# Performance work log

Hardware: AMD Instinct MI355X
Metric: run time of the kernel (lower is better)

The kernel has to match this reference:

```python
import jax, jax.numpy as jnp
import numpy as np

N_NODES = 100000

def sage_conv(x, src, dst, Wl, bl, Wr):
    # mean aggregation of source features at destination nodes
    msg = x[src]                                        # [E, d] gather
    agg = jax.ops.segment_sum(msg, dst, num_segments=N_NODES)
    deg = jax.ops.segment_sum(jnp.ones((src.shape[0],), x.dtype), dst, num_segments=N_NODES)
    agg = agg / jnp.maximum(deg, 1.0)[:, None]
    return agg @ Wl.T + bl + x @ Wr.T


def setup_inputs() -> dict:
    key = jax.random.key(0)
    ks = jax.random.split(key, 8)
    F, H, C = 128, 128, 64
    E = 1600000
    x = jax.random.normal(ks[0], (N_NODES, F), dtype=jnp.float32)
    edge_index = jax.random.randint(ks[1], (2, E), 0, N_NODES, dtype=jnp.int64)
    s = 1.0 / np.sqrt(F)
    return {
        'x': x,
        'edge_index': edge_index,
        'W1l': jax.random.normal(ks[2], (H, F), dtype=jnp.float32) * s,
        'b1': jnp.zeros((H,), jnp.float32),
        'W1r': jax.random.normal(ks[3], (H, F), dtype=jnp.float32) * s,
        'W2l': jax.random.normal(ks[4], (C, H), dtype=jnp.float32) * s,
        'b2': jnp.zeros((C,), jnp.float32),
        'W2r': jax.random.normal(ks[5], (C, H), dtype=jnp.float32) * s,
    }


def reference(x, edge_index, W1l, b1, W1r, W2l, b2, W2r):
    src, dst = edge_index[0], edge_index[1]
    h = sage_conv(x, src, dst, W1l, b1, W1r)
    h = jax.nn.relu(h)
    # dropout is identity at inference (training=False)
    h = sage_conv(h, src, dst, W2l, b2, W2r)
    return jax.nn.log_softmax(h, axis=1)
```

## Files before the change

### kernel.cpp

```cpp
#include <hip/hip_runtime.h>
#include <hip/hip_bf16.h>

#define N_NODES 100000
#define NBUCKET 250
#define BUCKET_W 400
#define BK_EPT 14

typedef __attribute__((ext_vector_type(8))) short short8;
typedef __attribute__((ext_vector_type(8))) unsigned short u16x8;
typedef __attribute__((ext_vector_type(4))) unsigned short u16x4;
typedef __attribute__((ext_vector_type(4))) float floatx4;
typedef __attribute__((ext_vector_type(2))) float floatx2;

__device__ __forceinline__ float b2f(unsigned short u) {
    return __uint_as_float(((unsigned int)u) << 16);
}
__device__ __forceinline__ unsigned short f2b(float f) {
    unsigned int u = __float_as_uint(f);
    unsigned int r = u + 0x7FFFu + ((u >> 16) & 1u);
    return (unsigned short)(r >> 16);
}

__global__ __launch_bounds__(256) void prep_kernel(
    const float* __restrict__ x,
    const float* __restrict__ W1l, const float* __restrict__ W1r,
    const float* __restrict__ W2l, const float* __restrict__ W2r,
    unsigned short* __restrict__ xb, unsigned char* __restrict__ xq,
    unsigned short* __restrict__ Wc1f,
    unsigned short* __restrict__ W2lf, unsigned short* __restrict__ W2rf,
    int* __restrict__ bucketCursor, int pairCap)
{
    int blk = blockIdx.x;
    if (blk < 12500) {
        int tid = blk * 256 + threadIdx.x;
        float4 v = ((const float4*)x)[tid];
        u16x4 o;
        o.x = f2b(v.x); o.y = f2b(v.y); o.z = f2b(v.z); o.w = f2b(v.w);
        ((u16x4*)xb)[tid] = o;
        int p = 0;
        p = __builtin_amdgcn_cvt_pk_fp8_f32(v.x, v.y, p, false);
        p = __builtin_amdgcn_cvt_pk_fp8_f32(v.z, v.w, p, true);
        ((unsigned int*)xq)[tid] = (unsigned int)p;
    } else if (blk < 12692) {
        int tid = (blk - 12500) * 256 + threadIdx.x;
        if (tid < 32768) {
            int j = tid & 7, lane = (tid >> 3) & 63, t = (tid >> 9) & 7, ks = tid >> 12;
            int m = lane & 15, quad = lane >> 4;
            int row = t * 16 + m;
            int k = ks * 32 + quad * 8 + j;
            float v = (k < 128) ? W1l[row * 128 + k] : W1r[row * 128 + (k - 128)];
            Wc1f[tid] = f2b(v);
        } else if (tid < 40960) {
            int idx = tid - 32768;
            int j = idx & 7, lane = (idx >> 3) & 63, t = (idx >> 9) & 3, ks = idx >> 11;
            int m = lane & 15, quad = lane >> 4;
            int row = t * 16 + m;
            int k = ks * 32 + quad * 8 + j;
            W2lf[idx] = f2b(W2l[row * 128 + k]);
        } else if (tid < 49152) {
            int idx = tid - 40960;
            int j = idx & 7, lane = (idx >> 3) & 63, t = (idx >> 9) & 3, ks = idx >> 11;
            int m = lane & 15, quad = lane >> 4;
            int row = t * 16 + m;
            int k = ks * 32 + quad * 8 + j;
            W2rf[idx] = f2b(W2r[row * 128 + k]);
        }
    } else {
        if (threadIdx.x < NBUCKET)
            bucketCursor[threadIdx.x] = threadIdx.x * pairCap;
    }
}

__global__ __launch_bounds__(1024) void bucket_kernel(
    const int* __restrict__ src, const int* __restrict__ dst,
    int* __restrict__ bucketCursor, int2* __restrict__ pairs, int E)
{
    __shared__ int cnt[NBUCKET];
    __shared__ int base[NBUCKET];
    const int EPB = 1024 * BK_EPT;
    int e0 = blockIdx.x * EPB;
    for (int t = threadIdx.x; t < NBUCKET; t += 1024) cnt[t] = 0;
    __syncthreads();

    int es[BK_EPT], ed[BK_EPT], rk[BK_EPT], bk[BK_EPT];
    #pragma unroll
    for (int j = 0; j < BK_EPT; j++) {
        int i = e0 + j * 1024 + threadIdx.x;
        if (i < E) {
            es[j] = src[i];
            ed[j] = dst[i];
            bk[j] = ed[j] / BUCKET_W;
            rk[j] = atomicAdd(&cnt[bk[j]], 1);
        } else {
            bk[j] = -1;
        }
    }
    __syncthreads();
    for (int t = threadIdx.x; t < NBUCKET; t += 1024)
        base[t] = atomicAdd(&bucketCursor[t], cnt[t]);
    __syncthreads();

    #pragma unroll
    for (int j = 0; j < BK_EPT; j++) {
        if (bk[j] >= 0)
            pairs[(size_t)base[bk[j]] + rk[j]] = make_int2(es[j], ed[j]);
    }
}

__global__ __launch_bounds__(1024) void fill_kernel(
    const int2* __restrict__ pairs, const int* __restrict__ bucketCursor,
    int* __restrict__ edge_src, int2* __restrict__ nodeInfo, int pairCap)
{
    __shared__ int hist[BUCKET_W];
    __shared__ int off[BUCKET_W];
    __shared__ int cur[BUCKET_W];
    int b = blockIdx.x;
    int t = threadIdx.x;
    int base = b * pairCap;
    int cnt = bucketCursor[b] - base;
    int node0 = b * BUCKET_W;

    if (t < BUCKET_W) hist[t] = 0;
    __syncthreads();
    for (int i = t; i < cnt; i += 1024)
        atomicAdd(&hist[pairs[base + i].y - node0], 1);
    __syncthreads();

    if (t < BUCKET_W) off[t] = hist[t];
    __syncthreads();
    for (int o = 1; o < BUCKET_W; o <<= 1) {
        int v = 0;
        if (t < BUCKET_W && t >= o) v = off[t - o];
        __syncthreads();
        if (t < BUCKET_W && t >= o) off[t] += v;
        __syncthreads();
    }
    if (t < BUCKET_W) {
        int gb = base + off[t] - hist[t];
        cur[t] = gb;
        nodeInfo[node0 + t] = make_int2(gb, hist[t]);
    }
    __syncthreads();

    for (int i = t; i < cnt; i += 1024) {
        int2 p = pairs[base + i];
        int pos = atomicAdd(&cur[p.y - node0], 1);
        edge_src[pos] = p.x;
    }
}

__global__ __launch_bounds__(256) void gather_fp8_kernel(
    const unsigned char* __restrict__ xq, const int* __restrict__ edge_src,
    const int2* __restrict__ nodeInfo, unsigned short* __restrict__ aggOut)
{
    int tid = blockIdx.x * 256 + threadIdx.x;
    int node = tid >> 3;
    int q = tid & 7;
    int2 info = nodeInfo[node];
    int e = info.x, deg = info.y, end = info.x + deg;
    const uint4* f16 = (const uint4*)xq;

    float acc[16];
    #pragma unroll
    for (int j = 0; j < 16; j++) acc[j] = 0.0f;

    #define ACC16(W)  do {                                                   \
        floatx2 p;                                                           \
        p = __builtin_amdgcn_cvt_pk_f32_fp8((W).x, false); acc[0]+=p.x; acc[1]+=p.y;  \
        p = __builtin_amdgcn_cvt_pk_f32_fp8((W).x, true);  acc[2]+=p.x; acc[3]+=p.y;  \
        p = __builtin_amdgcn_cvt_pk_f32_fp8((W).y, false); acc[4]+=p.x; acc[5]+=p.y;  \
        p = __builtin_amdgcn_cvt_pk_f32_fp8((W).y, true);  acc[6]+=p.x; acc[7]+=p.y;  \
        p = __builtin_amdgcn_cvt_pk_f32_fp8((W).z, false); acc[8]+=p.x; acc[9]+=p.y;  \
        p = __builtin_amdgcn_cvt_pk_f32_fp8((W).z, true);  acc[10]+=p.x; acc[11]+=p.y;\
        p = __builtin_amdgcn_cvt_pk_f32_fp8((W).w, false); acc[12]+=p.x; acc[13]+=p.y;\
        p = __builtin_amdgcn_cvt_pk_f32_fp8((W).w, true);  acc[14]+=p.x; acc[15]+=p.y;\
    } while (0)

    for (; e + 4 <= end; e += 4) {
        int s0 = edge_src[e + 0];
        int s1 = edge_src[e + 1];
        int s2 = edge_src[e + 2];
        int s3 = edge_src[e + 3];
        uint4 w0 = f16[(size_t)s0 * 8 + q];
        uint4 w1 = f16[(size_t)s1 * 8 + q];
        uint4 w2 = f16[(size_t)s2 * 8 + q];
        uint4 w3 = f16[(size_t)s3 * 8 + q];
        ACC16(w0); ACC16(w1); ACC16(w2); ACC16(w3);
    }
    for (; e < end; e++) {
        uint4 w0 = f16[(size_t)edge_src[e] * 8 + q];
        ACC16(w0);
    }
    #undef ACC16

    float inv = (deg > 0) ? 1.0f / (float)deg : 0.0f;
    u16x8 o0, o1;
    #pragma unroll
    for (int j = 0; j < 8; j++) { o0[j] = f2b(acc[j] * inv); o1[j] = f2b(acc[8 + j] * inv); }
    u16x8* op = (u16x8*)(aggOut + (size_t)node * 128 + q * 16);
    op[0] = o0;
    op[1] = o1;
}

__global__ __launch_bounds__(256, 2) void fused_l1_kernel(
    const unsigned short* __restrict__ a1b, const unsigned short* __restrict__ xb,
    const unsigned short* __restrict__ Wc1f, const float* __restrict__ b1,
    const unsigned short* __restrict__ W2lf, const unsigned short* __restrict__ W2rf,
    unsigned char* __restrict__ g2q, unsigned short* __restrict__ r2b)
{
    __shared__ unsigned short h_lds[4][32][136];

    int wave = threadIdx.x >> 6;
    int lane = threadIdx.x & 63;
    int m    = lane & 15;
    int quad = lane >> 4;
    int node0 = blockIdx.x * 128 + wave * 32;

    int n0 = min(node0 + m,      N_NODES - 1);
    int n1 = min(node0 + 16 + m, N_NODES - 1);

    short8 a0[8], a1[8];
    #pragma unroll
    for (int ks = 0; ks < 8; ks++) {
        int k0 = ks * 32 + quad * 8;
        const unsigned short* s = (ks < 4) ? a1b : xb;
        int koff = (ks < 4) ? k0 : (k0 - 128);
        a0[ks] = *(const short8*)(s + (size_t)n0 * 128 + koff);
        a1[ks] = *(const short8*)(s + (size_t)n1 * 128 + koff);
    }

    floatx4 acc[2][8];
    #pragma unroll
    for (int mt = 0; mt < 2; mt++)
        #pragma unroll
        for (int t = 0; t < 8; t++) acc[mt][t] = (floatx4)(0.0f);

    const unsigned short* Wp = Wc1f + (lane << 3);
    short8 bb[2][8];
    #pragma unroll
    for (int t = 0; t < 8; t++)
        bb[0][t] = *(const short8*)(Wp + ((t * 64) << 3));

    #pragma unroll
    for (int ks = 0; ks < 8; ks++) {
        if (ks < 7) {
            #pragma unroll
            for (int t = 0; t < 8; t++)
                bb[(ks + 1) & 1][t] =
                    *(const short8*)(Wp + ((((ks + 1) * 8 + t) * 64) << 3));
        }
        #pragma unroll
        for (int t = 0; t < 8; t++) {
            acc[0][t] = __builtin_amdgcn_mfma_f32_16x16x32_bf16(a0[ks], bb[ks & 1][t], acc[0][t], 0, 0, 0);
            acc[1][t] = __builtin_amdgcn_mfma_f32_16x16x32_bf16(a1[ks], bb[ks & 1][t], acc[1][t], 0, 0, 0);
        }
    }

    #pragma unroll
    for (int t = 0; t < 8; t++) {
        int j = t * 16 + m;
        float bias = b1[j];
        #pragma unroll
        for (int mt = 0; mt < 2; mt++) {
            #pragma unroll
            for (int r = 0; r < 4; r++) {
                int row = mt * 16 + quad * 4 + r;
                h_lds[wave][row][j] = f2b(fmaxf(acc[mt][t][r] + bias, 0.0f));
            }
        }
    }
    asm volatile("s_waitcnt lgkmcnt(0)" ::: "memory");

    short8 h0[4], h1[4];
    #pragma unroll
    for (int ks = 0; ks < 4; ks++) {
        int k0 = ks * 32 + quad * 8;
        h0[ks] = *(const short8*)&h_lds[wave][m][k0];
        h1[ks] = *(const short8*)&h_lds[wave][16 + m][k0];
    }

    floatx4 acc2[2][4], acc3[2][4];
    #pragma unroll
    for (int mt = 0; mt < 2; mt++)
        #pragma unroll
        for (int t = 0; t < 4; t++) { acc2[mt][t] = (floatx4)(0.0f); acc3[mt][t] = (floatx4)(0.0f); }

    const unsigned short* W2lp = W2lf + (lane << 3);
    const unsigned short* W2rp = W2rf + (lane << 3);
    short8 bl2[2][4], br2[2][4];
    #pragma unroll
    for (int t = 0; t < 4; t++) {
        bl2[0][t] = *(const short8*)(W2lp + ((t * 64) << 3));
        br2[0][t] = *(const short8*)(W2rp + ((t * 64) << 3));
    }

    #pragma unroll
    for (int ks = 0; ks < 4; ks++) {
        if (ks < 3) {
            #pragma unroll
            for (int t = 0; t < 4; t++) {
                bl2[(ks + 1) & 1][t] = *(const short8*)(W2lp + ((((ks + 1) * 4 + t) * 64) << 3));
                br2[(ks + 1) & 1][t] = *(const short8*)(W2rp + ((((ks + 1) * 4 + t) * 64) << 3));
            }
        }
        #pragma unroll
        for (int t = 0; t < 4; t++) {
            acc2[0][t] = __builtin_amdgcn_mfma_f32_16x16x32_bf16(h0[ks], bl2[ks & 1][t], acc2[0][t], 0, 0, 0);
            acc2[1][t] = __builtin_amdgcn_mfma_f32_16x16x32_bf16(h1[ks], bl2[ks & 1][t], acc2[1][t], 0, 0, 0);
            acc3[0][t] = __builtin_amdgcn_mfma_f32_16x16x32_bf16(h0[ks], br2[ks & 1][t], acc3[0][t], 0, 0, 0);
            acc3[1][t] = __builtin_amdgcn_mfma_f32_16x16x32_bf16(h1[ks], br2[ks & 1][t], acc3[1][t], 0, 0, 0);
        }
    }

    #pragma unroll
    for (int mt = 0; mt < 2; mt++) {
        #pragma unroll
        for (int r = 0; r < 4; r++) {
            int n = node0 + mt * 16 + quad * 4 + r;
            if (n < N_NODES) {
                int p = 0;
                p = __builtin_amdgcn_cvt_pk_fp8_f32(acc2[mt][0][r], acc2[mt][1][r], p, false);
                p = __builtin_amdgcn_cvt_pk_fp8_f32(acc2[mt][2][r], acc2[mt][3][r], p, true);
                *(unsigned int*)(g2q + (size_t)n * 64 + m * 4) = (unsigned int)p;
                u16x4 rb;
                rb.x = f2b(acc3[mt][0][r]);
                rb.y = f2b(acc3[mt][1][r]);
                rb.z = f2b(acc3[mt][2][r]);
                rb.w = f2b(acc3[mt][3][r]);
                *(u16x4*)(r2b + (size_t)n * 64 + m * 4) = rb;
            }
        }
    }
}

__global__ __launch_bounds__(256) void gather_final_kernel(
    const unsigned char* __restrict__ g2q, const int* __restrict__ edge_src,
    const int2* __restrict__ nodeInfo, const unsigned short* __restrict__ r2b,
    const float* __restrict__ b2, float* __restrict__ out)
{
    int tid = blockIdx.x * 256 + threadIdx.x;
    int node = tid >> 3;
    int q = tid & 7;
    int2 info = nodeInfo[node];
    int e = info.x, deg = info.y, end = info.x + deg;
    const uint2* f8 = (const uint2*)g2q;
    float acc[8];
    #pragma unroll
    for (int j = 0; j < 8; j++) acc[j] = 0.0f;

    #define ACC8(W)  do {                                                    \
        floatx2 p;                                                           \
        p = __builtin_amdgcn_cvt_pk_f32_fp8((W).x, false); acc[0]+=p.x; acc[1]+=p.y; \
        p = __builtin_amdgcn_cvt_pk_f32_fp8((W).x, true);  acc[2]+=p.x; acc[3]+=p.y; \
        p = __builtin_amdgcn_cvt_pk_f32_fp8((W).y, false); acc[4]+=p.x; acc[5]+=p.y; \
        p = __builtin_amdgcn_cvt_pk_f32_fp8((W).y, true);  acc[6]+=p.x; acc[7]+=p.y; \
    } while (0)

    for (; e + 4 <= end; e += 4) {
        int s0 = edge_src[e + 0];
        int s1 = edge_src[e + 1];
        int s2 = edge_src[e + 2];
        int s3 = edge_src[e + 3];
        uint2 v0 = f8[(size_t)s0 * 8 + q];
        uint2 v1 = f8[(size_t)s1 * 8 + q];
        uint2 v2 = f8[(size_t)s2 * 8 + q];
        uint2 v3 = f8[(size_t)s3 * 8 + q];
        ACC8(v0); ACC8(v1); ACC8(v2); ACC8(v3);
    }
    for (; e < end; e++) {
        uint2 v0 = f8[(size_t)edge_src[e] * 8 + q];
        ACC8(v0);
    }
    #undef ACC8

    float inv = (deg > 0) ? 1.0f / (float)deg : 0.0f;

    u16x8 rv = ((const u16x8*)r2b)[tid];

    float2 bb0 = *(const float2*)(b2 + 0  + 2 * q);
    float2 bb1 = *(const float2*)(b2 + 16 + 2 * q);
    float2 bb2 = *(const float2*)(b2 + 32 + 2 * q);
    float2 bb3 = *(const float2*)(b2 + 48 + 2 * q);

    float v[8];
    v[0] = acc[0] * inv + bb0.x + b2f(rv[0]);
    v[1] = acc[1] * inv + bb1.x + b2f(rv[1]);
    v[2] = acc[2] * inv + bb2.x + b2f(rv[2]);
    v[3] = acc[3] * inv + bb3.x + b2f(rv[3]);
    v[4] = acc[4] * inv + bb0.y + b2f(rv[4]);
    v[5] = acc[5] * inv + bb1.y + b2f(rv[5]);
    v[6] = acc[6] * inv + bb2.y + b2f(rv[6]);
    v[7] = acc[7] * inv + bb3.y + b2f(rv[7]);

    float mx = v[0];
    #pragma unroll
    for (int j = 1; j < 8; j++) mx = fmaxf(mx, v[j]);
    mx = fmaxf(mx, __shfl_xor(mx, 1, 64));
    mx = fmaxf(mx, __shfl_xor(mx, 2, 64));
    mx = fmaxf(mx, __shfl_xor(mx, 4, 64));
    float s = 0.0f;
    #pragma unroll
    for (int j = 0; j < 8; j++) s += expf(v[j] - mx);
    s += __shfl_xor(s, 1, 64);
    s += __shfl_xor(s, 2, 64);
    s += __shfl_xor(s, 4, 64);
    float lg = mx + logf(s);

    float* ob = out + (size_t)node * 64 + 2 * q;
    *(float2*)(ob + 0)  = make_float2(v[0] - lg, v[4] - lg);
    *(float2*)(ob + 16) = make_float2(v[1] - lg, v[5] - lg);
    *(float2*)(ob + 32) = make_float2(v[2] - lg, v[6] - lg);
    *(float2*)(ob + 48) = make_float2(v[3] - lg, v[7] - lg);
}

extern "C" void kernel_launch(void* const* d_in, const int* in_sizes, int n_in,
                              void* d_out, int out_size, void* d_ws, size_t ws_size,
                              hipStream_t stream)
{
    const float* x   = (const float*)d_in[0];
    const int*   ei  = (const int*)d_in[1];
    const float* W1l = (const float*)d_in[2];
    const float* b1  = (const float*)d_in[3];
    const float* W1r = (const float*)d_in[4];
    const float* W2l = (const float*)d_in[5];
    const float* b2  = (const float*)d_in[6];
    const float* W2r = (const float*)d_in[7];
    float* out = (float*)d_out;

    int E = in_sizes[1] / 2;
    const int* src = ei;
    const int* dst = ei + E;

    int pairCap = ((E / NBUCKET) * 3 / 2 + 255) / 256 * 256;

    char* ws = (char*)d_ws;
    int*  bucketCursor = (int*)ws;   ws += ((size_t)NBUCKET * 4 + 15) / 16 * 16;
    int2* pairs        = (int2*)ws;  ws += (size_t)NBUCKET * pairCap * 8;
    int*  edge_src     = (int*)ws;   ws += (size_t)NBUCKET * pairCap * 4;
    int2* nodeInfo     = (int2*)ws;  ws += (size_t)N_NODES * 8;
    unsigned short* xb   = (unsigned short*)ws;  ws += (size_t)N_NODES * 128 * 2;
    unsigned char*  xq   = (unsigned char*)ws;   ws += (size_t)N_NODES * 128;
    unsigned short* a1b  = (unsigned short*)ws;  ws += (size_t)N_NODES * 128 * 2;
    unsigned char*  g2q  = (unsigned char*)ws;   ws += (size_t)N_NODES * 64;
    unsigned short* r2b  = (unsigned short*)ws;  ws += (size_t)N_NODES * 64 * 2;
    unsigned short* Wc1f = (unsigned short*)ws;  ws += 128 * 256 * 2;
    unsigned short* W2lf = (unsigned short*)ws;  ws += 64 * 128 * 2;
    unsigned short* W2rf = (unsigned short*)ws;  ws += 64 * 128 * 2;

    prep_kernel<<<12693, 256, 0, stream>>>(
        x, W1l, W1r, W2l, W2r, xb, xq, Wc1f, W2lf, W2rf, bucketCursor, pairCap);

    {
        const int EPB = 1024 * BK_EPT;
        bucket_kernel<<<(E + EPB - 1) / EPB, 1024, 0, stream>>>(
            src, dst, bucketCursor, pairs, E);
    }

    fill_kernel<<<NBUCKET, 1024, 0, stream>>>(
        pairs, bucketCursor, edge_src, nodeInfo, pairCap);

    gather_fp8_kernel<<<(N_NODES * 8) / 256, 256, 0, stream>>>(
        xq, edge_src, nodeInfo, a1b);

    fused_l1_kernel<<<(N_NODES + 127) / 128, 256, 0, stream>>>(
        a1b, xb, Wc1f, b1, W2lf, W2rf, g2q, r2b);

    gather_final_kernel<<<(N_NODES * 8) / 256, 256, 0, stream>>>(
        g2q, edge_src, nodeInfo, r2b, b2, out);
}
```

Before: 257.8 us.

## Sort edges by source stripe within each node and grid-stride gather kernels

The fill kernel now orders each destination node's edge list by source-node stripe (16 stripes of 6250 nodes), using a 6400-key histogram and a two-level prefix scan. The aim is for concurrently running gather threads to touch nearby source rows at the same time and get better L2 locality. Both gather kernels are also turned into grid-stride loops over 3125 tiles with 1024 persistent blocks, so that within each sweep blocks process nodes in a similar stripe order. The cost is a heavier fill kernel with more shared memory and barriers, and less parallelism in the gathers.

```diff
diff --git a/kernel.cpp b/kernel.cpp
--- a/kernel.cpp
+++ b/kernel.cpp
@@ -5,6 +5,10 @@
 #define NBUCKET 250
 #define BUCKET_W 400
 #define BK_EPT 14
+#define NSTRIPE 16
+#define STRIPE_W 6250
+#define GATHER_TILES 3125
+#define GATHER_BLOCKS 1024
 
 typedef __attribute__((ext_vector_type(8))) short short8;
 typedef __attribute__((ext_vector_type(8))) unsigned short u16x8;
@@ -111,40 +115,58 @@
     const int2* __restrict__ pairs, const int* __restrict__ bucketCursor,
     int* __restrict__ edge_src, int2* __restrict__ nodeInfo, int pairCap)
 {
-    __shared__ int hist[BUCKET_W];
-    __shared__ int off[BUCKET_W];
-    __shared__ int cur[BUCKET_W];
+    const int NKEY = BUCKET_W * NSTRIPE;
+    __shared__ int hist[BUCKET_W * NSTRIPE];
+    __shared__ int offx[BUCKET_W * NSTRIPE];
+    __shared__ int psum[1024];
     int b = blockIdx.x;
     int t = threadIdx.x;
     int base = b * pairCap;
     int cnt = bucketCursor[b] - base;
     int node0 = b * BUCKET_W;
 
-    if (t < BUCKET_W) hist[t] = 0;
-    __syncthreads();
-    for (int i = t; i < cnt; i += 1024)
-        atomicAdd(&hist[pairs[base + i].y - node0], 1);
-    __syncthreads();
-
-    if (t < BUCKET_W) off[t] = hist[t];
-    __syncthreads();
-    for (int o = 1; o < BUCKET_W; o <<= 1) {
-        int v = 0;
-        if (t < BUCKET_W && t >= o) v = off[t - o];
-        __syncthreads();
-        if (t < BUCKET_W && t >= o) off[t] += v;
-        __syncthreads();
-    }
-    if (t < BUCKET_W) {
-        int gb = base + off[t] - hist[t];
-        cur[t] = gb;
-        nodeInfo[node0 + t] = make_int2(gb, hist[t]);
-    }
-    __syncthreads();
-
+    for (int k = t; k < NKEY; k += 1024) hist[k] = 0;
+    __syncthreads();
     for (int i = t; i < cnt; i += 1024) {
         int2 p = pairs[base + i];
-        int pos = atomicAdd(&cur[p.y - node0], 1);
+        int key = (p.y - node0) * NSTRIPE + p.x / STRIPE_W;
+        atomicAdd(&hist[key], 1);
+    }
+    __syncthreads();
+
+    int loc[8];
+    int mysum = 0;
+    if (t < 800) {
+        #pragma unroll
+        for (int j = 0; j < 8; j++) { loc[j] = mysum; mysum += hist[t * 8 + j]; }
+    }
+    psum[t] = mysum;
+    __syncthreads();
+    for (int o = 1; o < 1024; o <<= 1) {
+        int v = (t >= o) ? psum[t - o] : 0;
+        __syncthreads();
+        psum[t] += v;
+        __syncthreads();
+    }
+    int texcl = psum[t] - mysum;
+    if (t < 800) {
+        #pragma unroll
+        for (int j = 0; j < 8; j++) offx[t * 8 + j] = texcl + loc[j];
+    }
+    __syncthreads();
+
+    if (t < BUCKET_W) {
+        int beg = offx[t * NSTRIPE];
+        int nxt = (t == BUCKET_W - 1) ? cnt : offx[(t + 1) * NSTRIPE];
+        nodeInfo[node0 + t] = make_int2(base + beg, nxt - beg);
+    }
+    for (int k = t; k < NKEY; k += 1024) hist[k] = base + offx[k];
+    __syncthreads();
+
+    for (int i = t; i < cnt; i += 1024) {
+        int2 p = pairs[base + i];
+        int key = (p.y - node0) * NSTRIPE + p.x / STRIPE_W;
+        int pos = atomicAdd(&hist[key], 1);
         edge_src[pos] = p.x;
     }
 }
@@ -153,53 +175,55 @@
     const unsigned char* __restrict__ xq, const int* __restrict__ edge_src,
     const int2* __restrict__ nodeInfo, unsigned short* __restrict__ aggOut)
 {
-    int tid = blockIdx.x * 256 + threadIdx.x;
-    int node = tid >> 3;
-    int q = tid & 7;
-    int2 info = nodeInfo[node];
-    int e = info.x, deg = info.y, end = info.x + deg;
-    const uint4* f16 = (const uint4*)xq;
-
-    float acc[16];
-    #pragma unroll
-    for (int j = 0; j < 16; j++) acc[j] = 0.0f;
-
-    #define ACC16(W)  do {                                                   \
-        floatx2 p;                                                           \
-        p = __builtin_amdgcn_cvt_pk_f32_fp8((W).x, false); acc[0]+=p.x; acc[1]+=p.y;  \
-        p = __builtin_amdgcn_cvt_pk_f32_fp8((W).x, true);  acc[2]+=p.x; acc[3]+=p.y;  \
-        p = __builtin_amdgcn_cvt_pk_f32_fp8((W).y, false); acc[4]+=p.x; acc[5]+=p.y;  \
-        p = __builtin_amdgcn_cvt_pk_f32_fp8((W).y, true);  acc[6]+=p.x; acc[7]+=p.y;  \
-        p = __builtin_amdgcn_cvt_pk_f32_fp8((W).z, false); acc[8]+=p.x; acc[9]+=p.y;  \
-        p = __builtin_amdgcn_cvt_pk_f32_fp8((W).z, true);  acc[10]+=p.x; acc[11]+=p.y;\
-        p = __builtin_amdgcn_cvt_pk_f32_fp8((W).w, false); acc[12]+=p.x; acc[13]+=p.y;\
-        p = __builtin_amdgcn_cvt_pk_f32_fp8((W).w, true);  acc[14]+=p.x; acc[15]+=p.y;\
-    } while (0)
-
-    for (; e + 4 <= end; e += 4) {
-        int s0 = edge_src[e + 0];
-        int s1 = edge_src[e + 1];
-        int s2 = edge_src[e + 2];
-        int s3 = edge_src[e + 3];
-        uint4 w0 = f16[(size_t)s0 * 8 + q];
-        uint4 w1 = f16[(size_t)s1 * 8 + q];
-        uint4 w2 = f16[(size_t)s2 * 8 + q];
-        uint4 w3 = f16[(size_t)s3 * 8 + q];
-        ACC16(w0); ACC16(w1); ACC16(w2); ACC16(w3);
-    }
-    for (; e < end; e++) {
-        uint4 w0 = f16[(size_t)edge_src[e] * 8 + q];
-        ACC16(w0);
-    }
-    #undef ACC16
-
-    float inv = (deg > 0) ? 1.0f / (float)deg : 0.0f;
-    u16x8 o0, o1;
-    #pragma unroll
-    for (int j = 0; j < 8; j++) { o0[j] = f2b(acc[j] * inv); o1[j] = f2b(acc[8 + j] * inv); }
-    u16x8* op = (u16x8*)(aggOut + (size_t)node * 128 + q * 16);
-    op[0] = o0;
-    op[1] = o1;
+    for (int tile = blockIdx.x; tile < GATHER_TILES; tile += gridDim.x) {
+        int tid = tile * 256 + threadIdx.x;
+        int node = tid >> 3;
+        int q = tid & 7;
+        int2 info = nodeInfo[node];
+        int e = info.x, deg = info.y, end = info.x + deg;
+        const uint4* f16 = (const uint4*)xq;
+
+        float acc[16];
+        #pragma unroll
+        for (int j = 0; j < 16; j++) acc[j] = 0.0f;
+
+        #define ACC16(W)  do {                                                   \
+            floatx2 p;                                                           \
+            p = __builtin_amdgcn_cvt_pk_f32_fp8((W).x, false); acc[0]+=p.x; acc[1]+=p.y;  \
+            p = __builtin_amdgcn_cvt_pk_f32_fp8((W).x, true);  acc[2]+=p.x; acc[3]+=p.y;  \
+            p = __builtin_amdgcn_cvt_pk_f32_fp8((W).y, false); acc[4]+=p.x; acc[5]+=p.y;  \
+            p = __builtin_amdgcn_cvt_pk_f32_fp8((W).y, true);  acc[6]+=p.x; acc[7]+=p.y;  \
+            p = __builtin_amdgcn_cvt_pk_f32_fp8((W).z, false); acc[8]+=p.x; acc[9]+=p.y;  \
+            p = __builtin_amdgcn_cvt_pk_f32_fp8((W).z, true);  acc[10]+=p.x; acc[11]+=p.y;\
+            p = __builtin_amdgcn_cvt_pk_f32_fp8((W).w, false); acc[12]+=p.x; acc[13]+=p.y;\
+            p = __builtin_amdgcn_cvt_pk_f32_fp8((W).w, true);  acc[14]+=p.x; acc[15]+=p.y;\
+        } while (0)
+
+        for (; e + 4 <= end; e += 4) {
+            int s0 = edge_src[e + 0];
+            int s1 = edge_src[e + 1];
+            int s2 = edge_src[e + 2];
+            int s3 = edge_src[e + 3];
+            uint4 w0 = f16[(size_t)s0 * 8 + q];
+            uint4 w1 = f16[(size_t)s1 * 8 + q];
+            uint4 w2 = f16[(size_t)s2 * 8 + q];
+            uint4 w3 = f16[(size_t)s3 * 8 + q];
+            ACC16(w0); ACC16(w1); ACC16(w2); ACC16(w3);
+        }
+        for (; e < end; e++) {
+            uint4 w0 = f16[(size_t)edge_src[e] * 8 + q];
+            ACC16(w0);
+        }
+        #undef ACC16
+
+        float inv = (deg > 0) ? 1.0f / (float)deg : 0.0f;
+        u16x8 o0, o1;
+        #pragma unroll
+        for (int j = 0; j < 8; j++) { o0[j] = f2b(acc[j] * inv); o1[j] = f2b(acc[8 + j] * inv); }
+        u16x8* op = (u16x8*)(aggOut + (size_t)node * 128 + q * 16);
+        op[0] = o0;
+        op[1] = o1;
+    }
 }
 
 __global__ __launch_bounds__(256, 2) void fused_l1_kernel(
@@ -338,79 +362,81 @@
     const int2* __restrict__ nodeInfo, const unsigned short* __restrict__ r2b,
     const float* __restrict__ b2, float* __restrict__ out)
 {
-    int tid = blockIdx.x * 256 + threadIdx.x;
-    int node = tid >> 3;
-    int q = tid & 7;
-    int2 info = nodeInfo[node];
-    int e = info.x, deg = info.y, end = info.x + deg;
-    const uint2* f8 = (const uint2*)g2q;
-    float acc[8];
-    #pragma unroll
-    for (int j = 0; j < 8; j++) acc[j] = 0.0f;
-
-    #define ACC8(W)  do {                                                    \
-        floatx2 p;                                                           \
-        p = __builtin_amdgcn_cvt_pk_f32_fp8((W).x, false); acc[0]+=p.x; acc[1]+=p.y; \
-        p = __builtin_amdgcn_cvt_pk_f32_fp8((W).x, true);  acc[2]+=p.x; acc[3]+=p.y; \
-        p = __builtin_amdgcn_cvt_pk_f32_fp8((W).y, false); acc[4]+=p.x; acc[5]+=p.y; \
-        p = __builtin_amdgcn_cvt_pk_f32_fp8((W).y, true);  acc[6]+=p.x; acc[7]+=p.y; \
-    } while (0)
-
-    for (; e + 4 <= end; e += 4) {
-        int s0 = edge_src[e + 0];
-        int s1 = edge_src[e + 1];
-        int s2 = edge_src[e + 2];
-        int s3 = edge_src[e + 3];
-        uint2 v0 = f8[(size_t)s0 * 8 + q];
-        uint2 v1 = f8[(size_t)s1 * 8 + q];
-        uint2 v2 = f8[(size_t)s2 * 8 + q];
-        uint2 v3 = f8[(size_t)s3 * 8 + q];
-        ACC8(v0); ACC8(v1); ACC8(v2); ACC8(v3);
-    }
-    for (; e < end; e++) {
-        uint2 v0 = f8[(size_t)edge_src[e] * 8 + q];
-        ACC8(v0);
-    }
-    #undef ACC8
-
-    float inv = (deg > 0) ? 1.0f / (float)deg : 0.0f;
-
-    u16x8 rv = ((const u16x8*)r2b)[tid];
-
-    float2 bb0 = *(const float2*)(b2 + 0  + 2 * q);
-    float2 bb1 = *(const float2*)(b2 + 16 + 2 * q);
-    float2 bb2 = *(const float2*)(b2 + 32 + 2 * q);
-    float2 bb3 = *(const float2*)(b2 + 48 + 2 * q);
-
-    float v[8];
-    v[0] = acc[0] * inv + bb0.x + b2f(rv[0]);
-    v[1] = acc[1] * inv + bb1.x + b2f(rv[1]);
-    v[2] = acc[2] * inv + bb2.x + b2f(rv[2]);
-    v[3] = acc[3] * inv + bb3.x + b2f(rv[3]);
-    v[4] = acc[4] * inv + bb0.y + b2f(rv[4]);
-    v[5] = acc[5] * inv + bb1.y + b2f(rv[5]);
-    v[6] = acc[6] * inv + bb2.y + b2f(rv[6]);
-    v[7] = acc[7] * inv + bb3.y + b2f(rv[7]);
-
-    float mx = v[0];
-    #pragma unroll
-    for (int j = 1; j < 8; j++) mx = fmaxf(mx, v[j]);
-    mx = fmaxf(mx, __shfl_xor(mx, 1, 64));
-    mx = fmaxf(mx, __shfl_xor(mx, 2, 64));
-    mx = fmaxf(mx, __shfl_xor(mx, 4, 64));
-    float s = 0.0f;
-    #pragma unroll
-    for (int j = 0; j < 8; j++) s += expf(v[j] - mx);
-    s += __shfl_xor(s, 1, 64);
-    s += __shfl_xor(s, 2, 64);
-    s += __shfl_xor(s, 4, 64);
-    float lg = mx + logf(s);
-
-    float* ob = out + (size_t)node * 64 + 2 * q;
-    *(float2*)(ob + 0)  = make_float2(v[0] - lg, v[4] - lg);
-    *(float2*)(ob + 16) = make_float2(v[1] - lg, v[5] - lg);
-    *(float2*)(ob + 32) = make_float2(v[2] - lg, v[6] - lg);
-    *(float2*)(ob + 48) = make_float2(v[3] - lg, v[7] - lg);
+    for (int tile = blockIdx.x; tile < GATHER_TILES; tile += gridDim.x) {
+        int tid = tile * 256 + threadIdx.x;
+        int node = tid >> 3;
+        int q = tid & 7;
+        int2 info = nodeInfo[node];
+        int e = info.x, deg = info.y, end = info.x + deg;
+        const uint2* f8 = (const uint2*)g2q;
+        float acc[8];
+        #pragma unroll
+        for (int j = 0; j < 8; j++) acc[j] = 0.0f;
+
+        #define ACC8(W)  do {                                                    \
+            floatx2 p;                                                           \
+            p = __builtin_amdgcn_cvt_pk_f32_fp8((W).x, false); acc[0]+=p.x; acc[1]+=p.y; \
+            p = __builtin_amdgcn_cvt_pk_f32_fp8((W).x, true);  acc[2]+=p.x; acc[3]+=p.y; \
+            p = __builtin_amdgcn_cvt_pk_f32_fp8((W).y, false); acc[4]+=p.x; acc[5]+=p.y; \
+            p = __builtin_amdgcn_cvt_pk_f32_fp8((W).y, true);  acc[6]+=p.x; acc[7]+=p.y; \
+        } while (0)
+
+        for (; e + 4 <= end; e += 4) {
+            int s0 = edge_src[e + 0];
+            int s1 = edge_src[e + 1];
+            int s2 = edge_src[e + 2];
+            int s3 = edge_src[e + 3];
+            uint2 v0 = f8[(size_t)s0 * 8 + q];
+            uint2 v1 = f8[(size_t)s1 * 8 + q];
+            uint2 v2 = f8[(size_t)s2 * 8 + q];
+            uint2 v3 = f8[(size_t)s3 * 8 + q];
+            ACC8(v0); ACC8(v1); ACC8(v2); ACC8(v3);
+        }
+        for (; e < end; e++) {
+            uint2 v0 = f8[(size_t)edge_src[e] * 8 + q];
+            ACC8(v0);
+        }
+        #undef ACC8
+
+        float inv = (deg > 0) ? 1.0f / (float)deg : 0.0f;
+
+        u16x8 rv = ((const u16x8*)r2b)[tid];
+
+        float2 bb0 = *(const float2*)(b2 + 0  + 2 * q);
+        float2 bb1 = *(const float2*)(b2 + 16 + 2 * q);
+        float2 bb2 = *(const float2*)(b2 + 32 + 2 * q);
+        float2 bb3 = *(const float2*)(b2 + 48 + 2 * q);
+
+        float v[8];
+        v[0] = acc[0] * inv + bb0.x + b2f(rv[0]);
+        v[1] = acc[1] * inv + bb1.x + b2f(rv[1]);
+        v[2] = acc[2] * inv + bb2.x + b2f(rv[2]);
+        v[3] = acc[3] * inv + bb3.x + b2f(rv[3]);
+        v[4] = acc[4] * inv + bb0.y + b2f(rv[4]);
+        v[5] = acc[5] * inv + bb1.y + b2f(rv[5]);
+        v[6] = acc[6] * inv + bb2.y + b2f(rv[6]);
+        v[7] = acc[7] * inv + bb3.y + b2f(rv[7]);
+
+        float mx = v[0];
+        #pragma unroll
+        for (int j = 1; j < 8; j++) mx = fmaxf(mx, v[j]);
+        mx = fmaxf(mx, __shfl_xor(mx, 1, 64));
+        mx = fmaxf(mx, __shfl_xor(mx, 2, 64));
+        mx = fmaxf(mx, __shfl_xor(mx, 4, 64));
+        float s = 0.0f;
+        #pragma unroll
+        for (int j = 0; j < 8; j++) s += expf(v[j] - mx);
+        s += __shfl_xor(s, 1, 64);
+        s += __shfl_xor(s, 2, 64);
+        s += __shfl_xor(s, 4, 64);
+        float lg = mx + logf(s);
+
+        float* ob = out + (size_t)node * 64 + 2 * q;
+        *(float2*)(ob + 0)  = make_float2(v[0] - lg, v[4] - lg);
+        *(float2*)(ob + 16) = make_float2(v[1] - lg, v[5] - lg);
+        *(float2*)(ob + 32) = make_float2(v[2] - lg, v[6] - lg);
+        *(float2*)(ob + 48) = make_float2(v[3] - lg, v[7] - lg);
+    }
 }
 
 extern "C" void kernel_launch(void* const* d_in, const int* in_sizes, int n_in,
@@ -459,12 +485,12 @@
     fill_kernel<<<NBUCKET, 1024, 0, stream>>>(
         pairs, bucketCursor, edge_src, nodeInfo, pairCap);
 
-    gather_fp8_kernel<<<(N_NODES * 8) / 256, 256, 0, stream>>>(
+    gather_fp8_kernel<<<GATHER_BLOCKS, 256, 0, stream>>>(
         xq, edge_src, nodeInfo, a1b);
 
     fused_l1_kernel<<<(N_NODES + 127) / 128, 256, 0, stream>>>(
         a1b, xb, Wc1f, b1, W2lf, W2rf, g2q, r2b);
 
-    gather_final_kernel<<<(N_NODES * 8) / 256, 256, 0, stream>>>(
+    gather_final_kernel<<<GATHER_BLOCKS, 256, 0, stream>>>(
         g2q, edge_src, nodeInfo, r2b, b2, out);
 }
```

Result: slower. 265.6 us (+3.0%).

## Sort nodes by degree within buckets to balance gather warp work

Applied to the files above, without the earlier changes.

The fill kernel now builds a per-bucket counting sort of nodes by in-degree (capped at 63) and writes a worklist. Both gather kernels map threads to nodes through this worklist, so nodes in the same wavefront have similar degrees, which reduces divergence and idle lanes in the edge loops. The cost is an extra indirection load per thread, scattered output and residual reads (aggOut and r2b indexed by permuted node), and a little extra scan work in fill_kernel.

```diff
diff --git a/kernel.cpp b/kernel.cpp
--- a/kernel.cpp
+++ b/kernel.cpp
@@ -109,11 +109,14 @@
 
 __global__ __launch_bounds__(1024) void fill_kernel(
     const int2* __restrict__ pairs, const int* __restrict__ bucketCursor,
-    int* __restrict__ edge_src, int2* __restrict__ nodeInfo, int pairCap)
+    int* __restrict__ edge_src, int2* __restrict__ nodeInfo,
+    int* __restrict__ worklist, int pairCap)
 {
     __shared__ int hist[BUCKET_W];
     __shared__ int off[BUCKET_W];
     __shared__ int cur[BUCKET_W];
+    __shared__ int dh[64];
+    __shared__ int dex[64];
     int b = blockIdx.x;
     int t = threadIdx.x;
     int base = b * pairCap;
@@ -121,6 +124,7 @@
     int node0 = b * BUCKET_W;
 
     if (t < BUCKET_W) hist[t] = 0;
+    if (t >= BUCKET_W && t < BUCKET_W + 64) dh[t - BUCKET_W] = 0;
     __syncthreads();
     for (int i = t; i < cnt; i += 1024)
         atomicAdd(&hist[pairs[base + i].y - node0], 1);
@@ -139,6 +143,23 @@
         int gb = base + off[t] - hist[t];
         cur[t] = gb;
         nodeInfo[node0 + t] = make_int2(gb, hist[t]);
+        atomicAdd(&dh[min(hist[t], 63)], 1);
+    }
+    __syncthreads();
+
+    if (t < 64) dex[t] = dh[t];
+    __syncthreads();
+    for (int o = 1; o < 64; o <<= 1) {
+        int v = (t < 64 && t >= o) ? dex[t - o] : 0;
+        __syncthreads();
+        if (t < 64) dex[t] += v;
+        __syncthreads();
+    }
+    if (t < 64) dh[t] = dex[t] - dh[t];
+    __syncthreads();
+    if (t < BUCKET_W) {
+        int pos = atomicAdd(&dh[min(hist[t], 63)], 1);
+        worklist[node0 + pos] = node0 + t;
     }
     __syncthreads();
 
@@ -151,11 +172,12 @@
 
 __global__ __launch_bounds__(256) void gather_fp8_kernel(
     const unsigned char* __restrict__ xq, const int* __restrict__ edge_src,
-    const int2* __restrict__ nodeInfo, unsigned short* __restrict__ aggOut)
-{
-    int tid = blockIdx.x * 256 + threadIdx.x;
-    int node = tid >> 3;
-    int q = tid & 7;
+    const int2* __restrict__ nodeInfo, const int* __restrict__ worklist,
+    unsigned short* __restrict__ aggOut)
+{
+    int gid = blockIdx.x * 256 + threadIdx.x;
+    int node = worklist[gid >> 3];
+    int q = gid & 7;
     int2 info = nodeInfo[node];
     int e = info.x, deg = info.y, end = info.x + deg;
     const uint4* f16 = (const uint4*)xq;
@@ -335,12 +357,13 @@
 
 __global__ __launch_bounds__(256) void gather_final_kernel(
     const unsigned char* __restrict__ g2q, const int* __restrict__ edge_src,
-    const int2* __restrict__ nodeInfo, const unsigned short* __restrict__ r2b,
+    const int2* __restrict__ nodeInfo, const int* __restrict__ worklist,
+    const unsigned short* __restrict__ r2b,
     const float* __restrict__ b2, float* __restrict__ out)
 {
-    int tid = blockIdx.x * 256 + threadIdx.x;
-    int node = tid >> 3;
-    int q = tid & 7;
+    int gid = blockIdx.x * 256 + threadIdx.x;
+    int node = worklist[gid >> 3];
+    int q = gid & 7;
     int2 info = nodeInfo[node];
     int e = info.x, deg = info.y, end = info.x + deg;
     const uint2* f8 = (const uint2*)g2q;
@@ -375,7 +398,7 @@
 
     float inv = (deg > 0) ? 1.0f / (float)deg : 0.0f;
 
-    u16x8 rv = ((const u16x8*)r2b)[tid];
+    u16x8 rv = ((const u16x8*)r2b)[node * 8 + q];
 
     float2 bb0 = *(const float2*)(b2 + 0  + 2 * q);
     float2 bb1 = *(const float2*)(b2 + 16 + 2 * q);
@@ -438,6 +461,7 @@
     int2* pairs        = (int2*)ws;  ws += (size_t)NBUCKET * pairCap * 8;
     int*  edge_src     = (int*)ws;   ws += (size_t)NBUCKET * pairCap * 4;
     int2* nodeInfo     = (int2*)ws;  ws += (size_t)N_NODES * 8;
+    int*  worklist     = (int*)ws;   ws += (size_t)N_NODES * 4;
     unsigned short* xb   = (unsigned short*)ws;  ws += (size_t)N_NODES * 128 * 2;
     unsigned char*  xq   = (unsigned char*)ws;   ws += (size_t)N_NODES * 128;
     unsigned short* a1b  = (unsigned short*)ws;  ws += (size_t)N_NODES * 128 * 2;
@@ -457,14 +481,14 @@
     }
 
     fill_kernel<<<NBUCKET, 1024, 0, stream>>>(
-        pairs, bucketCursor, edge_src, nodeInfo, pairCap);
+        pairs, bucketCursor, edge_src, nodeInfo, worklist, pairCap);
 
     gather_fp8_kernel<<<(N_NODES * 8) / 256, 256, 0, stream>>>(
-        xq, edge_src, nodeInfo, a1b);
+        xq, edge_src, nodeInfo, worklist, a1b);
 
     fused_l1_kernel<<<(N_NODES + 127) / 128, 256, 0, stream>>>(
         a1b, xb, Wc1f, b1, W2lf, W2rf, g2q, r2b);
 
     gather_final_kernel<<<(N_NODES * 8) / 256, 256, 0, stream>>>(
-        g2q, edge_src, nodeInfo, r2b, b2, out);
-}
+        g2q, edge_src, nodeInfo, worklist, r2b, b2, out);
+}
```

New measurement: 268.2 us. 1.04x slower.

## Slice fp8 features into column-chunk planes for per-slice gather blocks

Applied to the files above, without the earlier changes.

Stores the fp8 copy of x and the layer-1 aggregate as eight 16-column planes (plane-major, node-minor), not row-major. Each gather block now handles one 16-byte column slice for 256 nodes, so each block's random reads fall in a 1.6 MB plane that caches better, and the aggregate stores are coalesced. The layer-1 fused kernel is updated to read A operands from the planar layout. The cost is that each node's edge list and nodeInfo are now read by eight separate blocks rather than eight adjacent lanes.

```diff
diff --git a/kernel.cpp b/kernel.cpp
--- a/kernel.cpp
+++ b/kernel.cpp
@@ -5,6 +5,7 @@
 #define NBUCKET 250
 #define BUCKET_W 400
 #define BK_EPT 14
+#define GFP8_GRID (((N_NODES + 255) / 256) * 8)
 
 typedef __attribute__((ext_vector_type(8))) short short8;
 typedef __attribute__((ext_vector_type(8))) unsigned short u16x8;
@@ -37,10 +38,13 @@
         u16x4 o;
         o.x = f2b(v.x); o.y = f2b(v.y); o.z = f2b(v.z); o.w = f2b(v.w);
         ((u16x4*)xb)[tid] = o;
+        int node = tid >> 5;
+        int j = tid & 31;
         int p = 0;
         p = __builtin_amdgcn_cvt_pk_fp8_f32(v.x, v.y, p, false);
         p = __builtin_amdgcn_cvt_pk_fp8_f32(v.z, v.w, p, true);
-        ((unsigned int*)xq)[tid] = (unsigned int)p;
+        ((unsigned int*)xq)[((size_t)(j >> 2) * N_NODES + node) * 4 + (j & 3)] =
+            (unsigned int)p;
     } else if (blk < 12692) {
         int tid = (blk - 12500) * 256 + threadIdx.x;
         if (tid < 32768) {
@@ -153,12 +157,12 @@
     const unsigned char* __restrict__ xq, const int* __restrict__ edge_src,
     const int2* __restrict__ nodeInfo, unsigned short* __restrict__ aggOut)
 {
-    int tid = blockIdx.x * 256 + threadIdx.x;
-    int node = tid >> 3;
-    int q = tid & 7;
+    int q = blockIdx.x & 7;
+    int node = (blockIdx.x >> 3) * 256 + threadIdx.x;
+    if (node >= N_NODES) return;
     int2 info = nodeInfo[node];
     int e = info.x, deg = info.y, end = info.x + deg;
-    const uint4* f16 = (const uint4*)xq;
+    const uint4* f16 = (const uint4*)xq + (size_t)q * N_NODES;
 
     float acc[16];
     #pragma unroll
@@ -181,14 +185,14 @@
         int s1 = edge_src[e + 1];
         int s2 = edge_src[e + 2];
         int s3 = edge_src[e + 3];
-        uint4 w0 = f16[(size_t)s0 * 8 + q];
-        uint4 w1 = f16[(size_t)s1 * 8 + q];
-        uint4 w2 = f16[(size_t)s2 * 8 + q];
-        uint4 w3 = f16[(size_t)s3 * 8 + q];
+        uint4 w0 = f16[s0];
+        uint4 w1 = f16[s1];
+        uint4 w2 = f16[s2];
+        uint4 w3 = f16[s3];
         ACC16(w0); ACC16(w1); ACC16(w2); ACC16(w3);
     }
     for (; e < end; e++) {
-        uint4 w0 = f16[(size_t)edge_src[e] * 8 + q];
+        uint4 w0 = f16[edge_src[e]];
         ACC16(w0);
     }
     #undef ACC16
@@ -197,7 +201,7 @@
     u16x8 o0, o1;
     #pragma unroll
     for (int j = 0; j < 8; j++) { o0[j] = f2b(acc[j] * inv); o1[j] = f2b(acc[8 + j] * inv); }
-    u16x8* op = (u16x8*)(aggOut + (size_t)node * 128 + q * 16);
+    u16x8* op = (u16x8*)(aggOut + ((size_t)q * N_NODES + node) * 16);
     op[0] = o0;
     op[1] = o1;
 }
@@ -222,11 +226,16 @@
     short8 a0[8], a1[8];
     #pragma unroll
     for (int ks = 0; ks < 8; ks++) {
-        int k0 = ks * 32 + quad * 8;
-        const unsigned short* s = (ks < 4) ? a1b : xb;
-        int koff = (ks < 4) ? k0 : (k0 - 128);
-        a0[ks] = *(const short8*)(s + (size_t)n0 * 128 + koff);
-        a1[ks] = *(const short8*)(s + (size_t)n1 * 128 + koff);
+        if (ks < 4) {
+            int q   = ks * 2 + (quad >> 1);
+            int rem = (quad & 1) * 8;
+            a0[ks] = *(const short8*)(a1b + ((size_t)q * N_NODES + n0) * 16 + rem);
+            a1[ks] = *(const short8*)(a1b + ((size_t)q * N_NODES + n1) * 16 + rem);
+        } else {
+            int koff = ks * 32 + quad * 8 - 128;
+            a0[ks] = *(const short8*)(xb + (size_t)n0 * 128 + koff);
+            a1[ks] = *(const short8*)(xb + (size_t)n1 * 128 + koff);
+        }
     }
 
     floatx4 acc[2][8];
@@ -459,7 +468,7 @@
     fill_kernel<<<NBUCKET, 1024, 0, stream>>>(
         pairs, bucketCursor, edge_src, nodeInfo, pairCap);
 
-    gather_fp8_kernel<<<(N_NODES * 8) / 256, 256, 0, stream>>>(
+    gather_fp8_kernel<<<GFP8_GRID, 256, 0, stream>>>(
         xq, edge_src, nodeInfo, a1b);
 
     fused_l1_kernel<<<(N_NODES + 127) / 128, 256, 0, stream>>>(
```

New measurement: 281.1 us. 1.09x slower.
